# Kernel tuning notes

Measured on AMD Instinct MI355X. Metric: run time of the kernel, lower is better.

The kernel has to match this reference:

```python
import jax, jax.numpy as jnp
import numpy as np
import math

N_HEADS = 8
EPS = 1e-12


def _ln(x, g, b):
    m = x.mean(-1, keepdims=True)
    v = ((x - m) ** 2).mean(-1, keepdims=True)
    return (x - m) * jax.lax.rsqrt(v + EPS) * g + b


def _ffn(x, w1, b1, w2, b2):
    # torch nn.GELU default = exact erf gelu; dropout is identity in eval
    return jax.nn.gelu(x @ w1 + b1, approximate=False) @ w2 + b2


def _mha(q_in, kv, mask, qw, qb, kw, kb, vw, vb, ow, ob):
    B, S, _ = q_in.shape
    dh = qw.shape[1] // N_HEADS

    def split(x):
        return x.reshape(B, S, N_HEADS, dh).transpose(0, 2, 1, 3)  # (B,H,S,dh)

    q = split(q_in @ qw + qb) / math.sqrt(dh)
    k = split(kv @ kw + kb)
    v = split(kv @ vw + vb)
    scores = jnp.einsum('bhqd,bhkd->bhqk', q, k) + mask[:, None]
    w = jax.nn.softmax(scores, axis=-1)
    ctx = jnp.einsum('bhqk,bhkd->bhqd', w, v)
    ctx = ctx.transpose(0, 2, 1, 3).reshape(B, S, N_HEADS * dh)
    return ctx @ ow + ob


def reference(hidden, lens,
              f_ffn_w1, f_ffn_b1, f_ffn_w2, f_ffn_b2, f_ln_g, f_ln_b,
              f_q_w, f_q_b, f_k_w, f_k_b, f_v_w, f_v_b, f_o_w, f_o_b,
              b_ffn_w1, b_ffn_b1, b_ffn_w2, b_ffn_b2, b_ln_g, b_ln_b,
              b_q_w, b_q_b, b_k_w, b_k_b, b_v_w, b_v_b, b_o_w, b_o_b,
              attn_ln_g, attn_ln_b,
              out_ffn_w1, out_ffn_b1, out_ffn_w2, out_ffn_b2,
              out_ln_g, out_ln_b):
    S, B, D2 = hidden.shape
    H = D2 // 2
    S2 = S - 2
    f = hidden[..., :H]
    bk = hidden[..., H:]
    query = jnp.concatenate([f[:-2], bk[2:]], axis=-1)        # (S2, B, 2H)
    qbf = jnp.swapaxes(query, 0, 1)                            # (B, S2, 2H)

    # vectorized per-sample length-dependent masks (additive, 0 / -inf)
    qi = jnp.arange(S2)[:, None]
    ki = jnp.arange(S2)[None, :]
    Lm = (lens - 2)[:, None, None]
    # forward: rows >= L-2 all zero; valid rows causal (k <= q) inside [0, L-2)
    f_mask = jnp.where((qi >= Lm) | (ki <= qi), 0.0, -np.inf).astype(hidden.dtype)
    # backward: rows >= L-2 all zero; valid rows anti-causal (k >= q) with k < L-2
    b_mask = jnp.where((qi >= Lm) | ((ki >= qi) & (ki < Lm)), 0.0, -np.inf).astype(hidden.dtype)

    f_q = _ln(_ffn(qbf, f_ffn_w1, f_ffn_b1, f_ffn_w2, f_ffn_b2), f_ln_g, f_ln_b)
    f_kv = jnp.swapaxes(f[:-2], 0, 1)
    f_attn = _mha(f_q, f_kv, f_mask, f_q_w, f_q_b, f_k_w, f_k_b, f_v_w, f_v_b, f_o_w, f_o_b)

    b_q = _ln(_ffn(qbf, b_ffn_w1, b_ffn_b1, b_ffn_w2, b_ffn_b2), b_ln_g, b_ln_b)
    b_kv = jnp.swapaxes(bk[2:], 0, 1)
    b_attn = _mha(b_q, b_kv, b_mask, b_q_w, b_q_b, b_k_w, b_k_b, b_v_w, b_v_b, b_o_w, b_o_b)

    attn_out = _ln(qbf + jnp.concatenate([f_attn, b_attn], axis=-1), attn_ln_g, attn_ln_b)
    out = _ln(_ffn(attn_out, out_ffn_w1, out_ffn_b1, out_ffn_w2, out_ffn_b2), out_ln_g, out_ln_b)
    return jnp.swapaxes(out, 0, 1)                             # (S2, B, 2H)


def setup_inputs():
    key = jax.random.key(0)
    ks = jax.random.split(key, 16)
    S, B, H = 1024, 8, 512
    d = {}
    d['hidden'] = jax.random.normal(ks[0], (S, B, 2 * H), jnp.float32)
    d['lens'] = jax.random.randint(ks[1], (B,), 4, S + 1)

    def w(k, i, o):
        return jax.random.normal(k, (i, o), jnp.float32) * 0.02

    idx = 2
    for p in ('f', 'b'):
        d[p + '_ffn_w1'] = w(ks[idx], 2 * H, 2 * H); idx += 1
        d[p + '_ffn_b1'] = jnp.zeros((2 * H,), jnp.float32)
        d[p + '_ffn_w2'] = w(ks[idx], 2 * H, H); idx += 1
        d[p + '_ffn_b2'] = jnp.zeros((H,), jnp.float32)
        d[p + '_ln_g'] = jnp.ones((H,), jnp.float32)
        d[p + '_ln_b'] = jnp.zeros((H,), jnp.float32)
        for n in ('q', 'k', 'v', 'o'):
            d[p + '_' + n + '_w'] = w(jax.random.fold_in(ks[idx], hash(n) % 97), H, H)
            d[p + '_' + n + '_b'] = jnp.zeros((H,), jnp.float32)
        idx += 1
    d['attn_ln_g'] = jnp.ones((2 * H,), jnp.float32)
    d['attn_ln_b'] = jnp.zeros((2 * H,), jnp.float32)
    d['out_ffn_w1'] = w(ks[idx], 2 * H, 2 * H); idx += 1
    d['out_ffn_b1'] = jnp.zeros((2 * H,), jnp.float32)
    d['out_ffn_w2'] = w(ks[idx], 2 * H, 2 * H); idx += 1
    d['out_ffn_b2'] = jnp.zeros((2 * H,), jnp.float32)
    d['out_ln_g'] = jnp.ones((2 * H,), jnp.float32)
    d['out_ln_b'] = jnp.zeros((2 * H,), jnp.float32)
    return d
```

## Files before the change

### kernel.cpp

```cpp
#include <hip/hip_runtime.h>
#include <cmath>

#define S_ 1024
#define B_ 8
#define H_ 512
#define S2_ 1022
#define M_ (B_*S2_)
#define PAD_ 8192
#define VTS_ ((size_t)8*8*64*1024)

typedef __attribute__((ext_vector_type(8))) short bf16x8;
typedef __attribute__((ext_vector_type(4))) float f32x4;
typedef __attribute__((ext_vector_type(4))) unsigned int u32x4;
typedef __attribute__((ext_vector_type(2))) unsigned int u32x2;

__device__ __forceinline__ unsigned short f2bf(float f){
  unsigned int u = __float_as_uint(f);
  return (unsigned short)((u + 0x7fffu + ((u>>16)&1u)) >> 16);
}
__device__ __forceinline__ float bf2f(unsigned short u){
  return __uint_as_float((unsigned int)u << 16);
}
__device__ __forceinline__ float fgelu(float x){
  float u = x * (0.7978845608f + 0.0356774081f * x * x);
  return x / (1.f + __expf(-2.f * u));
}
__device__ __forceinline__ float fexp2(float x){
  float r; asm("v_exp_f32 %0, %1" : "=v"(r) : "v"(x)); return r;
}
__device__ __forceinline__ unsigned int cvtpk(float lo, float hi){
  unsigned int r; asm("v_cvt_pk_bf16_f32 %0, %1, %2" : "=v"(r) : "v"(lo), "v"(hi)); return r;
}

__device__ __forceinline__ void glds16(const void* g, void* l){
  __builtin_amdgcn_global_load_lds((const __attribute__((address_space(1))) unsigned int*)g,
                                   (__attribute__((address_space(3))) unsigned int*)l, 16, 0, 0);
}
#define SB() __builtin_amdgcn_sched_barrier(0)

__global__ __launch_bounds__(256) void lma_prep_x(const float* __restrict__ hidden,
                                                  unsigned short* __restrict__ Xb){
  int m = blockIdx.x; int dq = threadIdx.x * 4;
  int b = m / S2_, s = m - b * S2_;
  int srow = (dq < 512) ? s : (s + 2);
  const float* src = hidden + ((size_t)srow * B_ + b) * 1024 + dq;
  f32x4 v = *(const f32x4*)src;
  union { u32x2 u; unsigned short s4[4]; } pk;
  #pragma unroll
  for (int j = 0; j < 4; j++) pk.s4[j] = f2bf(v[j]);
  *(u32x2*)&Xb[(size_t)m * 1024 + dq] = pk.u;
}

struct TPack {
  const float* src[14];
  unsigned short* dst[14];
  int K[14];
  int N[14];
};
__global__ __launch_bounds__(256) void lma_transpose_all(TPack p){
  int idx = blockIdx.z;
  int K = p.K[idx], N = p.N[idx];
  int kb = blockIdx.x * 32, nb = blockIdx.y * 32;
  if (kb >= K || nb >= N) return;
  const float* W = p.src[idx];
  unsigned short* WT = p.dst[idx];
  __shared__ float t[32][33];
  int tx = threadIdx.x & 31, ty = threadIdx.x >> 5;
  #pragma unroll
  for (int i = ty; i < 32; i += 8) t[i][tx] = W[(size_t)(kb + i) * N + nb + tx];
  __syncthreads();
  #pragma unroll
  for (int i = ty; i < 32; i += 8) WT[(size_t)(nb + i) * K + kb + tx] = f2bf(t[tx][i]);
}

__global__ __launch_bounds__(256) void lma_biascat(const float* __restrict__ fk, const float* __restrict__ fv,
                                                   const float* __restrict__ bk, const float* __restrict__ bv,
                                                   float* __restrict__ out){
  int i = blockIdx.x * 256 + threadIdx.x;
  int fb = i >> 10, col = i & 1023;
  const float* s = (col < 512) ? (fb ? bk : fk) : (fb ? bv : fv);
  out[i] = s[col & 511];
}

__global__ __launch_bounds__(256) void lma_vt2(const unsigned short* __restrict__ KV2,
                                               unsigned short* __restrict__ VT2){
  __shared__ unsigned short t[32][34];
  int s0 = blockIdx.x * 32, c0 = blockIdx.y * 32;
  int z = blockIdx.z, fb = z >> 3, b = z & 7;
  const unsigned short* V = KV2 + (size_t)fb * PAD_ * 1024 + 512;
  unsigned short* VT = VT2 + (size_t)fb * VTS_;
  int tx = threadIdx.x & 31, ty = threadIdx.x >> 5;
  #pragma unroll
  for (int i = ty; i < 32; i += 8){
    int s = s0 + i; if (s > S2_-1) s = S2_-1;
    t[i][tx] = V[((size_t)b * S2_ + s) * 1024 + c0 + tx];
  }
  __syncthreads();
  int s = s0 + tx;
  #pragma unroll
  for (int i = ty; i < 32; i += 8){
    int c = c0 + i, h = c >> 6, d = c & 63;
    VT[(((size_t)b * 8 + h) * 64 + d) * 1024 + s] = (s < S2_) ? t[tx][i] : (unsigned short)0;
  }
}

__global__ __launch_bounds__(256) void lma_gemm2(
    const unsigned short* __restrict__ A, int lda,
    const unsigned short* __restrict__ Bt0, const unsigned short* __restrict__ Bt1,
    const float* __restrict__ bias0, const float* __restrict__ bias1,
    void* __restrict__ Cout, int ldc,
    int M, int N, int K, int mode, int amap, int nmt)
{
  __shared__ unsigned short Al[128*32];
  __shared__ unsigned short Bl[128*32];
  const int tid = threadIdx.x;
  const int w = tid >> 6, lane = tid & 63, quad = lane >> 4, l16 = lane & 15;
  const int mt = blockIdx.x % nmt, nt = blockIdx.x / nmt;
  const int m0 = mt * 128, n0 = nt * 128;
  const int brch = m0 >> 13;
  const unsigned short* Bt = brch ? Bt1 : Bt0;
  const float* bias = brch ? bias1 : bias0;
  const int coloff = (amap == 2 && brch) ? 512 : 0;
  const int wm = (w >> 1) * 64, wn = (w & 1) * 64;

  f32x4 acc[4][4];
  #pragma unroll
  for (int i = 0; i < 4; i++)
    #pragma unroll
    for (int f = 0; f < 4; f++) acc[i][f] = f32x4{0.f,0.f,0.f,0.f};

  const int srow = lane >> 2;
  const int spc  = (((lane & 3) ^ ((lane >> 3) & 3))) * 8;
  const int rswz = (l16 >> 1) & 3;

  for (int k0 = 0; k0 < K; k0 += 32) {
    #pragma unroll
    for (int c = 0; c < 2; c++) {
      int ra = w*32 + c*16 + srow;
      int ga = m0 + ra;
      int ar;
      if (amap == 0) { ar = (ga > M-1) ? (M-1) : ga; }
      else { ar = ga & (PAD_-1); if (ar > M_-1) ar = M_-1; }
      glds16(A + (size_t)ar * lda + coloff + k0 + spc, &Al[(w*32 + c*16) * 32]);
      int gb = n0 + ra; if (gb > N-1) gb = N-1;
      glds16(Bt + (size_t)gb * K + k0 + spc, &Bl[(w*32 + c*16) * 32]);
    }
    __syncthreads();
    bf16x8 af[4], bfr[4];
    #pragma unroll
    for (int i = 0; i < 4; i++) af[i]  = *(const bf16x8*)&Al[(wm + i*16 + l16)*32 + ((quad ^ rswz) * 8)];
    #pragma unroll
    for (int f = 0; f < 4; f++) bfr[f] = *(const bf16x8*)&Bl[(wn + f*16 + l16)*32 + ((quad ^ rswz) * 8)];
    #pragma unroll
    for (int i = 0; i < 4; i++)
      #pragma unroll
      for (int f = 0; f < 4; f++)
        acc[i][f] = __builtin_amdgcn_mfma_f32_16x16x32_bf16(af[i], bfr[f], acc[i][f], 0, 0, 0);
    __syncthreads();
  }

  float bv[4];
  #pragma unroll
  for (int f = 0; f < 4; f++) bv[f] = bias ? bias[n0 + wn + f*16 + l16] : 0.f;
  const int col0 = n0 + wn + l16;
  #pragma unroll
  for (int i = 0; i < 4; i++) {
    #pragma unroll
    for (int r = 0; r < 4; r++) {
      int row = m0 + wm + i*16 + quad*4 + r;
      if (row < M) {
        #pragma unroll
        for (int f = 0; f < 4; f++) {
          float v = acc[i][f][r] + bv[f];
          if (mode == 2) v = fgelu(v);
          else if (mode == 1) v *= 0.18033688011112042f;
          if (mode <= 2) ((unsigned short*)Cout)[(size_t)row * ldc + col0 + f*16] = f2bf(v);
          else if (mode == 3) ((float*)Cout)[(size_t)row * ldc + col0 + f*16] = v;
          else {
            int sr = row % S2_, bb2 = row / S2_;
            ((float*)Cout)[((size_t)sr * B_ + bb2) * ldc + col0 + f*16] = v;
          }
        }
      }
    }
  }
}

__global__ __launch_bounds__(512, 2) void lma_gemm8(
    const unsigned short* __restrict__ A, int lda,
    const unsigned short* __restrict__ Bt0, const unsigned short* __restrict__ Bt1,
    const float* __restrict__ bias0, const float* __restrict__ bias1,
    unsigned short* __restrict__ Cout, int ldc,
    int M, int N, int K, int mode, int amap, int nmt)
{
  __shared__ unsigned short Ls[2][2][256*64];
  const int tid = threadIdx.x;
  const int w = tid >> 6, lane = tid & 63, quad = lane >> 4, l16 = lane & 15;
  const int mt = blockIdx.x % nmt, nt = blockIdx.x / nmt;
  const int m0 = mt * 256, n0 = nt * 256;
  const int brch = m0 >> 13;
  const unsigned short* Bt = brch ? Bt1 : Bt0;
  const float* bias = brch ? bias1 : bias0;
  const int coloff = (amap == 2 && brch) ? 512 : 0;
  const int wm = (w >> 2) * 128, wn = (w & 3) * 64;

  f32x4 acc[8][4];
  #pragma unroll
  for (int i = 0; i < 8; i++)
    #pragma unroll
    for (int f = 0; f < 4; f++) acc[i][f] = f32x4{0.f,0.f,0.f,0.f};

  const int lrow8 = lane >> 3;
  const int lkb   = lane & 7;
  const int NT = K >> 6;

  const unsigned short* aP[2][2]; const unsigned short* bP[2][2];
  int aD[2][2], bD[2][2];
  #pragma unroll
  for (int hf = 0; hf < 2; hf++)
    #pragma unroll
    for (int c = 0; c < 2; c++) {
      int rtA = (w>>2)*128 + hf*64 + ((w&3)*2 + c)*8 + lrow8;
      int kbA = lkb ^ (rtA & 7);
      int ga = m0 + rtA;
      int ar;
      if (amap == 0) { ar = (ga > M-1) ? (M-1) : ga; }
      else { ar = ga & (PAD_-1); if (ar > M_-1) ar = M_-1; }
      aP[hf][c] = A + (size_t)ar * lda + coloff + kbA*8;
      aD[hf][c] = ((w>>2)*128 + hf*64 + ((w&3)*2 + c)*8) * 64;
      int rtB = (w>>1)*64 + hf*32 + ((w&1)*2 + c)*8 + lrow8;
      int kbB = lkb ^ (rtB & 7);
      int gb = n0 + rtB; if (gb > N-1) gb = N-1;
      bP[hf][c] = Bt + (size_t)gb * K + kbB*8;
      bD[hf][c] = ((w>>1)*64 + hf*32 + ((w&1)*2 + c)*8) * 64;
    }

  bf16x8 af[4][2], bf[2][2];

  #define STA(buf, hf, kt) { _Pragma("unroll") for (int c = 0; c < 2; c++) \
      glds16(aP[hf][c] + (size_t)(kt)*64, &Ls[buf][0][aD[hf][c]]); }
  #define STB(buf, hf, kt) { _Pragma("unroll") for (int c = 0; c < 2; c++) \
      glds16(bP[hf][c] + (size_t)(kt)*64, &Ls[buf][1][bD[hf][c]]); }
  #define LDA8(buf, mq) { _Pragma("unroll") for (int j = 0; j < 4; j++){ \
      int rt = wm + (mq)*64 + j*16 + l16; \
      const unsigned short* base = &Ls[buf][0][rt*64]; \
      int f_ = rt & 7; \
      af[j][0] = *(const bf16x8*)(base + ((    quad) ^ f_)*8); \
      af[j][1] = *(const bf16x8*)(base + ((4 + quad) ^ f_)*8); } }
  #define LDB8(buf, nq) { _Pragma("unroll") for (int j = 0; j < 2; j++){ \
      int rt = wn + (nq)*32 + j*16 + l16; \
      const unsigned short* base = &Ls[buf][1][rt*64]; \
      int f_ = rt & 7; \
      bf[j][0] = *(const bf16x8*)(base + ((    quad) ^ f_)*8); \
      bf[j][1] = *(const bf16x8*)(base + ((4 + quad) ^ f_)*8); } }
  #define MFMAQ(mq, nq) { __builtin_amdgcn_s_setprio(1); \
      _Pragma("unroll") for (int j = 0; j < 4; j++) \
        _Pragma("unroll") for (int j2 = 0; j2 < 2; j2++){ \
          acc[(mq)*4+j][(nq)*2+j2] = __builtin_amdgcn_mfma_f32_16x16x32_bf16(af[j][0], bf[j2][0], acc[(mq)*4+j][(nq)*2+j2], 0, 0, 0); \
          acc[(mq)*4+j][(nq)*2+j2] = __builtin_amdgcn_mfma_f32_16x16x32_bf16(af[j][1], bf[j2][1], acc[(mq)*4+j][(nq)*2+j2], 0, 0, 0); } \
      __builtin_amdgcn_s_setprio(0); }
  #define BAR()   { SB(); __builtin_amdgcn_s_barrier(); SB(); }
  #define LGKM0() { asm volatile("s_waitcnt lgkmcnt(0)" ::: "memory"); SB(); }
  #define VM6()   { asm volatile("s_waitcnt vmcnt(6)"   ::: "memory"); SB(); }
  #define VM2()   { asm volatile("s_waitcnt vmcnt(2)"   ::: "memory"); SB(); }

  STA(0, 0, 0); STB(0, 0, 0); STB(0, 1, 0); STA(0, 1, 0);
  STA(1, 0, 1);
  asm volatile("s_waitcnt vmcnt(2)" ::: "memory"); SB();
  BAR();

  const int NI = NT >> 1;
  for (int i = 0; i < NI; i++) {
    const int tb  = 2*i + 1;
    int ta2 = 2*i + 2; if (ta2 > NT-1) ta2 = NT-1;
    int tb2 = 2*i + 3; if (tb2 > NT-1) tb2 = NT-1;

    LDA8(0, 0); LDB8(0, 0); STB(1, 0, tb);
    BAR(); LGKM0(); MFMAQ(0, 0); BAR();
    LDB8(0, 1); STB(1, 1, tb);
    BAR(); LGKM0(); MFMAQ(0, 1); BAR();
    LDA8(0, 1); STA(1, 1, tb);
    BAR(); LGKM0(); MFMAQ(1, 1); BAR();
    LDB8(0, 0); STA(0, 0, ta2);
    BAR(); LGKM0(); MFMAQ(1, 0); VM6(); BAR();
    LDA8(1, 0); LDB8(1, 0); STB(0, 1, ta2);
    BAR(); LGKM0(); MFMAQ(0, 0); VM6(); BAR();
    LDB8(1, 1); STA(0, 1, ta2);
    BAR(); LGKM0(); MFMAQ(0, 1); VM6(); BAR();
    LDA8(1, 1); STB(0, 0, ta2);
    BAR(); LGKM0(); MFMAQ(1, 1); BAR();
    LDB8(1, 0); STA(1, 0, tb2);
    BAR(); LGKM0(); MFMAQ(1, 0); VM2(); BAR();
  }
  asm volatile("s_waitcnt vmcnt(0)" ::: "memory");

  float bv[4];
  #pragma unroll
  for (int f = 0; f < 4; f++) bv[f] = bias ? bias[n0 + wn + f*16 + l16] : 0.f;
  const int col0 = n0 + wn + l16;
  #pragma unroll
  for (int i2 = 0; i2 < 8; i2++) {
    #pragma unroll
    for (int r = 0; r < 4; r++) {
      int row = m0 + wm + i2*16 + quad*4 + r;
      if (row < M) {
        #pragma unroll
        for (int f = 0; f < 4; f++) {
          float v = acc[i2][f][r] + bv[f];
          if (mode == 2) v = fgelu(v);
          Cout[(size_t)row * ldc + col0 + f*16] = f2bf(v);
        }
      }
    }
  }
  #undef STA
  #undef STB
  #undef LDA8
  #undef LDB8
  #undef MFMAQ
  #undef BAR
  #undef LGKM0
  #undef VM6
  #undef VM2
}

__device__ __forceinline__ void lma_red2(float& s, float& sq){
  __shared__ float red[16];
  #pragma unroll
  for (int msk = 1; msk < 64; msk <<= 1){ s += __shfl_xor(s, msk); sq += __shfl_xor(sq, msk); }
  int w = threadIdx.x >> 6;
  if ((threadIdx.x & 63) == 0){ red[w] = s; red[8 + w] = sq; }
  __syncthreads();
  s  = red[0] + red[1] + red[2] + red[3];
  sq = red[8] + red[9] + red[10] + red[11];
}

__global__ __launch_bounds__(256) void lma_ln(const float* __restrict__ in,
                                              const float* __restrict__ g, const float* __restrict__ bb,
                                              int D, unsigned short* __restrict__ obf, float* __restrict__ of32){
  int row = blockIdx.x, t = threadIdx.x;
  const float* x = in + (size_t)row * D;
  float s = 0.f, sq = 0.f;
  for (int d = t; d < D; d += 256){ float v = x[d]; s += v; sq += v * v; }
  lma_red2(s, sq);
  float mean = s / D;
  float var = sq / D - mean * mean;
  float rstd = rsqrtf(fmaxf(var, 0.f) + 1e-12f);
  if (obf) {
    for (int d = t; d < D; d += 256) obf[(size_t)row * D + d] = f2bf((x[d] - mean) * rstd * g[d] + bb[d]);
  } else {
    for (int d = t; d < D; d += 256) of32[(size_t)row * D + d] = (x[d] - mean) * rstd * g[d] + bb[d];
  }
}

__global__ __launch_bounds__(256) void lma_ln2(const unsigned short* __restrict__ T12b,
                                               const float* __restrict__ fg, const float* __restrict__ fbb,
                                               const float* __restrict__ bg, const float* __restrict__ bbb,
                                               unsigned short* __restrict__ LQ2){
  int m = blockIdx.x, t = threadIdx.x;
  int fb = (m >= M_);
  int idx = m - fb * M_;
  const float* g = fb ? bg : fg;
  const float* bb = fb ? bbb : fbb;
  const unsigned short* x = T12b + ((size_t)fb * PAD_ + idx) * 512;
  unsigned short* o = LQ2 + ((size_t)fb * PAD_ + idx) * 512;
  float v0 = bf2f(x[t]), v1 = bf2f(x[t + 256]);
  float s = v0 + v1, sq = v0*v0 + v1*v1;
  lma_red2(s, sq);
  float mean = s / 512.f;
  float var = sq / 512.f - mean * mean;
  float rstd = rsqrtf(fmaxf(var, 0.f) + 1e-12f);
  o[t]       = f2bf((v0 - mean) * rstd * g[t]       + bb[t]);
  o[t + 256] = f2bf((v1 - mean) * rstd * g[t + 256] + bb[t + 256]);
}

__global__ __launch_bounds__(256) void lma_attn_ln(const unsigned short* __restrict__ pf,
                                                   const unsigned short* __restrict__ pb,
                                                   const float* __restrict__ hidden,
                                                   const float* __restrict__ g, const float* __restrict__ bb,
                                                   unsigned short* __restrict__ out){
  int m = blockIdx.x, t = threadIdx.x;
  int b = m / S2_, s = m - b * S2_;
  const float* hf = hidden + ((size_t)s       * B_ + b) * 1024;
  const float* hb = hidden + ((size_t)(s + 2) * B_ + b) * 1024;
  float v[4]; float sum = 0.f, sq = 0.f;
  #pragma unroll
  for (int j = 0; j < 4; j++){
    int d = t + j * 256;
    float x = (d < 512) ? (bf2f(pf[(size_t)m * 512 + d]) + hf[d])
                        : (bf2f(pb[(size_t)m * 512 + (d - 512)]) + hb[d]);
    v[j] = x; sum += x; sq += x * x;
  }
  lma_red2(sum, sq);
  float mean = sum / 1024.f;
  float var = sq / 1024.f - mean * mean;
  float rstd = rsqrtf(fmaxf(var, 0.f) + 1e-12f);
  #pragma unroll
  for (int j = 0; j < 4; j++){
    int d = t + j * 256;
    out[(size_t)m * 1024 + d] = f2bf((v[j] - mean) * rstd * g[d] + bb[d]);
  }
}

__global__ __launch_bounds__(256, 4) void lma_attn9(const unsigned short* __restrict__ Q2,
                                                    const unsigned short* __restrict__ KV2,
                                                    const unsigned short* __restrict__ VT2,
                                                    unsigned short* __restrict__ CT2,
                                                    const int* __restrict__ lens,
                                                    int fb){
  __shared__ unsigned short Kl[64*64];
  __shared__ unsigned short Vl[64*64];
  __shared__ __align__(16) unsigned short Pl[4][16*64];

  const int tid = threadIdx.x;
  const int w = tid >> 6, lane = tid & 63, quad = lane >> 4, l16 = lane & 15;
  const int id = blockIdx.x;
  const int qt = id >> 6, h = (id >> 3) & 7, b = id & 7;
  const int backward = fb;
  const int L2 = lens[b] - 2;
  const int q0wg = qt * 64;
  const int q0 = q0wg + w * 16;
  const int qg = q0 + l16;
  const int qload = (qg > S2_-1) ? (S2_-1) : qg;

  const size_t qbase  = ((size_t)b * S2_) * 512  + h * 64;
  const size_t kbase  = ((size_t)b * S2_) * 1024 + h * 64;
  const size_t vtbase = ((size_t)(b * 8 + h) * 64) * 1024;
  char* Pb = (char*)&Pl[w][0];

  const int lrow = lane >> 3;
  const int g0s  = (lane & 7) ^ lrow;
  const int x7   = l16 & 7;
  const int x7s  = x7 << 4;

  const unsigned short* Q  = Q2  + (size_t)fb * PAD_ * 512;
  const unsigned short* Kx = KV2 + (size_t)fb * PAD_ * 1024;
  const unsigned short* VT = VT2 + (size_t)fb * VTS_;
  unsigned short* CTX      = CT2 + (size_t)fb * PAD_ * 512;

  bf16x8 qf[2];
  {
    const unsigned short* qp = Q + qbase + (size_t)qload * 512 + quad * 8;
    qf[0] = *(const bf16x8*)(qp);
    qf[1] = *(const bf16x8*)(qp + 32);
  }

  float mi = -3e38f, li = 0.f;
  f32x4 ot[4];
  #pragma unroll
  for (int f = 0; f < 4; f++) ot[f] = f32x4{0.f,0.f,0.f,0.f};

  int klo = 0, khi = S2_ - 1;
  if (q0wg + 63 < L2) {
    if (!backward) khi = q0wg + 63;
    else { klo = q0wg; khi = L2 - 1; }
  }

  for (int kt0 = klo; kt0 <= khi; kt0 += 64) {
    #pragma unroll
    for (int c = 0; c < 2; c++) {
      int r = w*16 + c*8 + lrow;
      int kr = kt0 + r; if (kr > S2_-1) kr = S2_-1;
      glds16(Kx + kbase + (size_t)kr * 1024 + g0s * 8, &Kl[(w*16 + c*8) * 64]);
      glds16(VT + vtbase + (size_t)r * 1024 + kt0 + g0s * 8, &Vl[(w*16 + c*8) * 64]);
    }
    __syncthreads();

    bf16x8 kf[4][2], vf[4][2];
    #pragma unroll
    for (int sub = 0; sub < 4; sub++) {
      const unsigned short* kp = &Kl[(sub*16 + l16) * 64];
      kf[sub][0] = *(const bf16x8*)(kp + (( quad      ^ x7) * 8));
      kf[sub][1] = *(const bf16x8*)(kp + (((quad + 4) ^ x7) * 8));
    }
    #pragma unroll
    for (int f = 0; f < 4; f++) {
      const unsigned short* vp = &Vl[(f*16 + l16) * 64];
      vf[f][0] = *(const bf16x8*)(vp + (( quad      ^ x7) * 8));
      vf[f][1] = *(const bf16x8*)(vp + (((quad + 4) ^ x7) * 8));
    }

    f32x4 st[4];
    __builtin_amdgcn_s_setprio(1);
    #pragma unroll
    for (int sub = 0; sub < 4; sub++) {
      f32x4 s = f32x4{0.f,0.f,0.f,0.f};
      s = __builtin_amdgcn_mfma_f32_16x16x32_bf16(kf[sub][0], qf[0], s, 0, 0, 0);
      s = __builtin_amdgcn_mfma_f32_16x16x32_bf16(kf[sub][1], qf[1], s, 0, 0, 0);
      st[sub] = s;
    }
    __builtin_amdgcn_s_setprio(0);

    {
      bool tail = (kt0 + 63 > S2_ - 1);
      bool full;
      if (!backward) full = !tail && ((kt0 + 63 <= q0) || (q0 >= L2));
      else           full = !tail && ((q0 >= L2) || ((kt0 >= q0 + 15) && (kt0 + 63 < L2)));
      if (!full) {
        #pragma unroll
        for (int sub = 0; sub < 4; sub++) {
          #pragma unroll
          for (int r = 0; r < 4; r++) {
            int kg = kt0 + sub*16 + quad*4 + r;
            bool ok;
            if (!backward) ok = (kg < S2_) && ((qg >= L2) || (kg <= qg));
            else           ok = (kg < S2_) && ((qg >= L2) || ((kg >= qg) && (kg < L2)));
            if (!ok) st[sub][r] = -3e38f;
          }
        }
      }
    }

    float mx = -3e38f;
    #pragma unroll
    for (int sub = 0; sub < 4; sub++)
      #pragma unroll
      for (int r = 0; r < 4; r++) mx = fmaxf(mx, st[sub][r]);
    mx = fmaxf(mx, __shfl_xor(mx, 16));
    mx = fmaxf(mx, __shfl_xor(mx, 32));

    if (__any(mx > mi + 11.f)) {
      float mn = fmaxf(mi, mx);
      float al = fexp2(mi - mn);
      li *= al;
      #pragma unroll
      for (int f = 0; f < 4; f++)
        #pragma unroll
        for (int r = 0; r < 4; r++) ot[f][r] *= al;
      mi = mn;
    }

    float rs = 0.f;
    #pragma unroll
    for (int sub = 0; sub < 4; sub++)
      #pragma unroll
      for (int r = 0; r < 4; r++) {
        float p = fexp2(st[sub][r] - mi);
        st[sub][r] = p; rs += p;
      }
    rs += __shfl_xor(rs, 16);
    rs += __shfl_xor(rs, 32);
    li += rs;

    #pragma unroll
    for (int sub = 0; sub < 4; sub++) {
      u32x2 pk2;
      pk2[0] = cvtpk(st[sub][0], st[sub][1]);
      pk2[1] = cvtpk(st[sub][2], st[sub][3]);
      *(u32x2*)(Pb + (l16*128 + ((sub*32 + quad*8) ^ x7s))) = pk2;
    }
    bf16x8 pfr0 = *(const bf16x8*)(Pb + (l16*128 + (( 0 + quad*16) ^ x7s)));
    bf16x8 pfr1 = *(const bf16x8*)(Pb + (l16*128 + ((64 + quad*16) ^ x7s)));

    __builtin_amdgcn_s_setprio(1);
    #pragma unroll
    for (int f = 0; f < 4; f++) {
      ot[f] = __builtin_amdgcn_mfma_f32_16x16x32_bf16(vf[f][0], pfr0, ot[f], 0, 0, 0);
      ot[f] = __builtin_amdgcn_mfma_f32_16x16x32_bf16(vf[f][1], pfr1, ot[f], 0, 0, 0);
    }
    __builtin_amdgcn_s_setprio(0);
    __syncthreads();
  }

  if (qg < S2_) {
    float rcp = 1.f / li;
    #pragma unroll
    for (int f = 0; f < 4; f++) {
      ushort4 pk;
      pk.x = f2bf(ot[f][0] * rcp); pk.y = f2bf(ot[f][1] * rcp);
      pk.z = f2bf(ot[f][2] * rcp); pk.w = f2bf(ot[f][3] * rcp);
      *(ushort4*)&CTX[qbase + (size_t)qg * 512 + f*16 + quad*4] = pk;
    }
  }
}

extern "C" void kernel_launch(void* const* d_in, const int* in_sizes, int n_in,
                              void* d_out, int out_size, void* d_ws, size_t ws_size,
                              hipStream_t stream)
{
  const float* hidden = (const float*)d_in[0];
  const int*   lens   = (const int*)d_in[1];
  const float* fw[14]; for (int i = 0; i < 14; i++) fw[i] = (const float*)d_in[2 + i];
  const float* bw[14]; for (int i = 0; i < 14; i++) bw[i] = (const float*)d_in[16 + i];
  const float* attn_g = (const float*)d_in[30];
  const float* attn_b = (const float*)d_in[31];
  const float* o_w1 = (const float*)d_in[32];
  const float* o_b1 = (const float*)d_in[33];
  const float* o_w2 = (const float*)d_in[34];
  const float* o_b2 = (const float*)d_in[35];
  const float* o_lng = (const float*)d_in[36];
  const float* o_lnb = (const float*)d_in[37];

  char* ws = (char*)d_ws;
  size_t off = 0;
  auto alloc = [&](size_t bytes)->char* {
    off = (off + 255) & ~(size_t)255;
    char* p = ws + off; off += bytes; return p;
  };

  unsigned short* fw1t = (unsigned short*)alloc((size_t)1024*1024*2);
  unsigned short* fw2t = (unsigned short*)alloc((size_t)512*1024*2);
  unsigned short* fqt  = (unsigned short*)alloc((size_t)512*512*2);
  unsigned short* fkvt = (unsigned short*)alloc((size_t)1024*512*2);
  unsigned short* fot  = (unsigned short*)alloc((size_t)512*512*2);
  unsigned short* bw1t = (unsigned short*)alloc((size_t)1024*1024*2);
  unsigned short* bw2t = (unsigned short*)alloc((size_t)512*1024*2);
  unsigned short* bqt  = (unsigned short*)alloc((size_t)512*512*2);
  unsigned short* bkvt = (unsigned short*)alloc((size_t)1024*512*2);
  unsigned short* bot  = (unsigned short*)alloc((size_t)512*512*2);
  unsigned short* ow1t = (unsigned short*)alloc((size_t)1024*1024*2);
  unsigned short* ow2t = (unsigned short*)alloc((size_t)1024*1024*2);
  float*          biasKV = (float*)alloc(2048*4);

  unsigned short* Xb   = (unsigned short*)alloc((size_t)M_*1024*2);
  unsigned short* big1 = (unsigned short*)alloc((size_t)2*PAD_*1024*2);
  float*          big2 = (float*)alloc((size_t)2*PAD_*512*4);
  unsigned short* LQCT = (unsigned short*)alloc((size_t)2*PAD_*512*2);
  unsigned short* Q2   = (unsigned short*)alloc((size_t)2*PAD_*512*2);

  unsigned short* H12 = big1, *KV2 = big1, *H1o = big1;
  unsigned short* T12b = (unsigned short*)big2;
  unsigned short* VT2  = (unsigned short*)big2;
  unsigned short* P2b  = (unsigned short*)big2 + 2*VTS_;
  unsigned short* LQ2 = LQCT, *CT2 = LQCT;

  lma_prep_x<<<M_, 256, 0, stream>>>(hidden, Xb);

  {
    TPack tp;
    const float* srcs[14] = { fw[0], fw[2], fw[6], fw[8], fw[10], fw[12],
                              bw[0], bw[2], bw[6], bw[8], bw[10], bw[12],
                              o_w1, o_w2 };
    unsigned short* dsts[14] = { fw1t, fw2t, fqt, fkvt, fkvt + (size_t)512*512, fot,
                                 bw1t, bw2t, bqt, bkvt, bkvt + (size_t)512*512, bot,
                                 ow1t, ow2t };
    int Ks[14] = {1024,1024,512,512,512,512, 1024,1024,512,512,512,512, 1024,1024};
    int Ns[14] = {1024, 512,512,512,512,512, 1024, 512,512,512,512,512, 1024,1024};
    for (int i = 0; i < 14; i++){ tp.src[i]=srcs[i]; tp.dst[i]=dsts[i]; tp.K[i]=Ks[i]; tp.N[i]=Ns[i]; }
    lma_transpose_all<<<dim3(32, 32, 14), 256, 0, stream>>>(tp);
  }
  lma_biascat<<<8, 256, 0, stream>>>(fw[9], fw[11], bw[9], bw[11], biasKV);

  auto G = [&](const unsigned short* A, int lda,
               const unsigned short* B0, const unsigned short* B1,
               const float* b0, const float* b1,
               void* C, int ldc, int M, int N, int K, int mode, int amap){
    int nmt = (M + 127) / 128;
    lma_gemm2<<<dim3(nmt * (N/128)), 256, 0, stream>>>(A, lda, B0, B1, b0, b1, C, ldc, M, N, K, mode, amap, nmt);
  };
  auto G8 = [&](const unsigned short* A, int lda,
                const unsigned short* B0, const unsigned short* B1,
                const float* b0, const float* b1,
                unsigned short* C, int ldc, int M, int N, int K, int mode, int amap){
    int nmt = M / 256;
    lma_gemm8<<<dim3(nmt * (N/256)), 512, 0, stream>>>(A, lda, B0, B1, b0, b1, C, ldc, M, N, K, mode, amap, nmt);
  };

  G8(Xb, 1024, fw1t, bw1t, fw[1], bw[1], H12, 1024, 2*PAD_, 1024, 1024, 2, 1);
  G(H12, 1024, fw2t, bw2t, fw[3], bw[3], T12b, 512, 2*PAD_, 512, 1024, 0, 0);
  lma_ln2<<<2*M_, 256, 0, stream>>>(T12b, fw[4], fw[5], bw[4], bw[5], LQ2);
  G(LQ2, 512, fqt, bqt, fw[7], bw[7], Q2, 512, 2*PAD_, 512, 512, 1, 0);
  G8(Xb, 1024, fkvt, bkvt, biasKV, biasKV + 1024, KV2, 1024, 2*PAD_, 1024, 512, 0, 2);
  lma_vt2<<<dim3(32, 16, 16), 256, 0, stream>>>(KV2, VT2);

  lma_attn9<<<dim3(1024), 256, 0, stream>>>(Q2, KV2, VT2, CT2, lens, 0);
  lma_attn9<<<dim3(1024), 256, 0, stream>>>(Q2, KV2, VT2, CT2, lens, 1);

  G(CT2, 512, fot, bot, fw[13], bw[13], P2b, 512, 2*PAD_, 512, 512, 0, 0);

  lma_attn_ln<<<M_, 256, 0, stream>>>(P2b, P2b + (size_t)PAD_*512, hidden, attn_g, attn_b, Xb);

  G(Xb, 1024, ow1t, ow1t, o_b1, o_b1, H1o, 1024, M_, 1024, 1024, 2, 0);
  G(H1o, 1024, ow2t, ow2t, o_b2, o_b2, (float*)d_out, 1024, M_, 1024, 1024, 4, 0);
  lma_ln<<<M_, 256, 0, stream>>>((float*)d_out, o_lng, o_lnb, 1024, nullptr, (float*)d_out);
}
```

Measured before the change: 568.9 us.

## Add 128x256 eight-wave GEMM kernel for remaining GEMMs and merge attention directions

Adds a new 512-thread GEMM kernel with 128x256 tiles, a double-buffered LDS pipeline and interleaved load/MFMA phases. It replaces the older 128x128 lma_gemm2 path for the FFN2, Q projection, output projection and output FFN GEMMs. Separately, forward and backward attention now run sequentially inside one launch instead of two. The wider tiles aim to raise operand reuse and per-block MFMA throughput, at the cost of higher register/LDS use per block. Serialising the two directions per block halves the grid's parallel work in exchange for one fewer launch.

Measured after the change: 550.8 us. 3.2% less time.

```diff
diff --git a/kernel.cpp b/kernel.cpp
--- a/kernel.cpp
+++ b/kernel.cpp
@@ -324,6 +324,146 @@
   #undef VM2
 }
 
+__global__ __launch_bounds__(512, 2) void lma_gemm8w(
+    const unsigned short* __restrict__ A, int lda,
+    const unsigned short* __restrict__ Bt0, const unsigned short* __restrict__ Bt1,
+    const float* __restrict__ bias0, const float* __restrict__ bias1,
+    void* __restrict__ Cout, int ldc,
+    int M, int N, int K, int mode, int nmt)
+{
+  __shared__ unsigned short LsA[2][128*64];
+  __shared__ unsigned short LsB[2][256*64];
+  const int tid = threadIdx.x;
+  const int w = tid >> 6, lane = tid & 63, quad = lane >> 4, l16 = lane & 15;
+  const int mt = blockIdx.x % nmt, nt = blockIdx.x / nmt;
+  const int m0 = mt * 128, n0 = nt * 256;
+  const int brch = m0 >> 13;
+  const unsigned short* Bt = brch ? Bt1 : Bt0;
+  const float* bias = brch ? bias1 : bias0;
+  const int wm = (w >> 2) * 64, wn = (w & 3) * 64;
+
+  f32x4 acc[4][4];
+  #pragma unroll
+  for (int i = 0; i < 4; i++)
+    #pragma unroll
+    for (int f = 0; f < 4; f++) acc[i][f] = f32x4{0.f,0.f,0.f,0.f};
+
+  const int lrow8 = lane >> 3;
+  const int lkb   = lane & 7;
+  const int NT = K >> 6;
+
+  const unsigned short* aP[2]; int aD[2];
+  const unsigned short* bP[2][2]; int bD[2][2];
+  #pragma unroll
+  for (int hf = 0; hf < 2; hf++) {
+    int rtA = hf*64 + w*8 + lrow8;
+    int kbA = lkb ^ (rtA & 7);
+    int ga = m0 + rtA; if (ga > M-1) ga = M-1;
+    aP[hf] = A + (size_t)ga * lda + kbA*8;
+    aD[hf] = (hf*64 + w*8) * 64;
+    #pragma unroll
+    for (int c = 0; c < 2; c++) {
+      int rtB = hf*128 + (w*2 + c)*8 + lrow8;
+      int kbB = lkb ^ (rtB & 7);
+      int gb = n0 + rtB; if (gb > N-1) gb = N-1;
+      bP[hf][c] = Bt + (size_t)gb * K + kbB*8;
+      bD[hf][c] = (hf*128 + (w*2 + c)*8) * 64;
+    }
+  }
+
+  bf16x8 af[2][2], bf[2][2];
+
+  #define WSTA(buf, hf, kt) { glds16(aP[hf] + (size_t)(kt)*64, &LsA[buf][aD[hf]]); }
+  #define WSTB(buf, hf, kt) { _Pragma("unroll") for (int c = 0; c < 2; c++) \
+      glds16(bP[hf][c] + (size_t)(kt)*64, &LsB[buf][bD[hf][c]]); }
+  #define WLDA(buf, mq) { _Pragma("unroll") for (int j = 0; j < 2; j++){ \
+      int rt = wm + (mq)*32 + j*16 + l16; \
+      const unsigned short* base = &LsA[buf][rt*64]; \
+      int f_ = rt & 7; \
+      af[j][0] = *(const bf16x8*)(base + ((    quad) ^ f_)*8); \
+      af[j][1] = *(const bf16x8*)(base + ((4 + quad) ^ f_)*8); } }
+  #define WLDB(buf, nq) { _Pragma("unroll") for (int j = 0; j < 2; j++){ \
+      int rt = wn + (nq)*32 + j*16 + l16; \
+      const unsigned short* base = &LsB[buf][rt*64]; \
+      int f_ = rt & 7; \
+      bf[j][0] = *(const bf16x8*)(base + ((    quad) ^ f_)*8); \
+      bf[j][1] = *(const bf16x8*)(base + ((4 + quad) ^ f_)*8); } }
+  #define WMFMAQ(mq, nq) { __builtin_amdgcn_s_setprio(1); \
+      _Pragma("unroll") for (int j = 0; j < 2; j++) \
+        _Pragma("unroll") for (int j2 = 0; j2 < 2; j2++){ \
+          acc[(mq)*2+j][(nq)*2+j2] = __builtin_amdgcn_mfma_f32_16x16x32_bf16(af[j][0], bf[j2][0], acc[(mq)*2+j][(nq)*2+j2], 0, 0, 0); \
+          acc[(mq)*2+j][(nq)*2+j2] = __builtin_amdgcn_mfma_f32_16x16x32_bf16(af[j][1], bf[j2][1], acc[(mq)*2+j][(nq)*2+j2], 0, 0, 0); } \
+      __builtin_amdgcn_s_setprio(0); }
+  #define WBAR()   { SB(); __builtin_amdgcn_s_barrier(); SB(); }
+  #define WLGKM0() { asm volatile("s_waitcnt lgkmcnt(0)" ::: "memory"); SB(); }
+  #define WVM4()   { asm volatile("s_waitcnt vmcnt(4)"   ::: "memory"); SB(); }
+  #define WVM1()   { asm volatile("s_waitcnt vmcnt(1)"   ::: "memory"); SB(); }
+
+  WSTA(0, 0, 0); WSTB(0, 0, 0); WSTB(0, 1, 0); WSTA(0, 1, 0);
+  WSTA(1, 0, 1);
+  WVM1(); WBAR();
+
+  const int NI = NT >> 1;
+  for (int i = 0; i < NI; i++) {
+    const int tb  = 2*i + 1;
+    int ta2 = 2*i + 2; if (ta2 > NT-1) ta2 = NT-1;
+    int tb2 = 2*i + 3; if (tb2 > NT-1) tb2 = NT-1;
+
+    WLDA(0, 0); WLDB(0, 0); WSTB(1, 0, tb);
+    WBAR(); WLGKM0(); WMFMAQ(0, 0); WBAR();
+    WLDB(0, 1); WSTB(1, 1, tb);
+    WBAR(); WLGKM0(); WMFMAQ(0, 1); WBAR();
+    WLDA(0, 1); WSTA(1, 1, tb);
+    WBAR(); WLGKM0(); WMFMAQ(1, 1); WBAR();
+    WLDB(0, 0); WSTA(0, 0, ta2);
+    WBAR(); WLGKM0(); WMFMAQ(1, 0); WVM4(); WBAR();
+    WLDA(1, 0); WLDB(1, 0); WSTB(0, 1, ta2);
+    WBAR(); WLGKM0(); WMFMAQ(0, 0); WVM4(); WBAR();
+    WLDB(1, 1); WSTA(0, 1, ta2);
+    WBAR(); WLGKM0(); WMFMAQ(0, 1); WVM4(); WBAR();
+    WLDA(1, 1); WSTB(0, 0, ta2);
+    WBAR(); WLGKM0(); WMFMAQ(1, 1); WBAR();
+    WLDB(1, 0); WSTA(1, 0, tb2);
+    WBAR(); WLGKM0(); WMFMAQ(1, 0); WVM1(); WBAR();
+  }
+  asm volatile("s_waitcnt vmcnt(0)" ::: "memory");
+
+  float bv[4];
+  #pragma unroll
+  for (int f = 0; f < 4; f++) bv[f] = bias ? bias[n0 + wn + f*16 + l16] : 0.f;
+  const int col0 = n0 + wn + l16;
+  #pragma unroll
+  for (int i2 = 0; i2 < 4; i2++) {
+    #pragma unroll
+    for (int r = 0; r < 4; r++) {
+      int row = m0 + wm + i2*16 + quad*4 + r;
+      if (row < M) {
+        #pragma unroll
+        for (int f = 0; f < 4; f++) {
+          float v = acc[i2][f][r] + bv[f];
+          if (mode == 2) v = fgelu(v);
+          else if (mode == 1) v *= 0.18033688011112042f;
+          if (mode <= 2) ((unsigned short*)Cout)[(size_t)row * ldc + col0 + f*16] = f2bf(v);
+          else if (mode == 3) ((float*)Cout)[(size_t)row * ldc + col0 + f*16] = v;
+          else {
+            int sr = row % S2_, bb2 = row / S2_;
+            ((float*)Cout)[((size_t)sr * B_ + bb2) * ldc + col0 + f*16] = v;
+          }
+        }
+      }
+    }
+  }
+  #undef WSTA
+  #undef WSTB
+  #undef WLDA
+  #undef WLDB
+  #undef WMFMAQ
+  #undef WBAR
+  #undef WLGKM0
+  #undef WVM4
+  #undef WVM1
+}
+
 __device__ __forceinline__ void lma_red2(float& s, float& sq){
   __shared__ float red[16];
   #pragma unroll
@@ -402,12 +542,11 @@
   }
 }
 
-__global__ __launch_bounds__(256, 4) void lma_attn9(const unsigned short* __restrict__ Q2,
-                                                    const unsigned short* __restrict__ KV2,
-                                                    const unsigned short* __restrict__ VT2,
-                                                    unsigned short* __restrict__ CT2,
-                                                    const int* __restrict__ lens,
-                                                    int fb){
+__global__ __launch_bounds__(256, 4) void lma_attn10(const unsigned short* __restrict__ Q2,
+                                                     const unsigned short* __restrict__ KV2,
+                                                     const unsigned short* __restrict__ VT2,
+                                                     unsigned short* __restrict__ CT2,
+                                                     const int* __restrict__ lens){
   __shared__ unsigned short Kl[64*64];
   __shared__ unsigned short Vl[64*64];
   __shared__ __align__(16) unsigned short Pl[4][16*64];
@@ -416,7 +555,6 @@
   const int w = tid >> 6, lane = tid & 63, quad = lane >> 4, l16 = lane & 15;
   const int id = blockIdx.x;
   const int qt = id >> 6, h = (id >> 3) & 7, b = id & 7;
-  const int backward = fb;
   const int L2 = lens[b] - 2;
   const int q0wg = qt * 64;
   const int q0 = q0wg + w * 16;
@@ -433,143 +571,146 @@
   const int x7   = l16 & 7;
   const int x7s  = x7 << 4;
 
-  const unsigned short* Q  = Q2  + (size_t)fb * PAD_ * 512;
-  const unsigned short* Kx = KV2 + (size_t)fb * PAD_ * 1024;
-  const unsigned short* VT = VT2 + (size_t)fb * VTS_;
-  unsigned short* CTX      = CT2 + (size_t)fb * PAD_ * 512;
-
-  bf16x8 qf[2];
-  {
-    const unsigned short* qp = Q + qbase + (size_t)qload * 512 + quad * 8;
-    qf[0] = *(const bf16x8*)(qp);
-    qf[1] = *(const bf16x8*)(qp + 32);
-  }
-
-  float mi = -3e38f, li = 0.f;
-  f32x4 ot[4];
-  #pragma unroll
-  for (int f = 0; f < 4; f++) ot[f] = f32x4{0.f,0.f,0.f,0.f};
-
-  int klo = 0, khi = S2_ - 1;
-  if (q0wg + 63 < L2) {
-    if (!backward) khi = q0wg + 63;
-    else { klo = q0wg; khi = L2 - 1; }
-  }
-
-  for (int kt0 = klo; kt0 <= khi; kt0 += 64) {
-    #pragma unroll
-    for (int c = 0; c < 2; c++) {
-      int r = w*16 + c*8 + lrow;
-      int kr = kt0 + r; if (kr > S2_-1) kr = S2_-1;
-      glds16(Kx + kbase + (size_t)kr * 1024 + g0s * 8, &Kl[(w*16 + c*8) * 64]);
-      glds16(VT + vtbase + (size_t)r * 1024 + kt0 + g0s * 8, &Vl[(w*16 + c*8) * 64]);
-    }
-    __syncthreads();
-
-    bf16x8 kf[4][2], vf[4][2];
-    #pragma unroll
-    for (int sub = 0; sub < 4; sub++) {
-      const unsigned short* kp = &Kl[(sub*16 + l16) * 64];
-      kf[sub][0] = *(const bf16x8*)(kp + (( quad      ^ x7) * 8));
-      kf[sub][1] = *(const bf16x8*)(kp + (((quad + 4) ^ x7) * 8));
-    }
-    #pragma unroll
-    for (int f = 0; f < 4; f++) {
-      const unsigned short* vp = &Vl[(f*16 + l16) * 64];
-      vf[f][0] = *(const bf16x8*)(vp + (( quad      ^ x7) * 8));
-      vf[f][1] = *(const bf16x8*)(vp + (((quad + 4) ^ x7) * 8));
-    }
-
-    f32x4 st[4];
-    __builtin_amdgcn_s_setprio(1);
-    #pragma unroll
-    for (int sub = 0; sub < 4; sub++) {
-      f32x4 s = f32x4{0.f,0.f,0.f,0.f};
-      s = __builtin_amdgcn_mfma_f32_16x16x32_bf16(kf[sub][0], qf[0], s, 0, 0, 0);
-      s = __builtin_amdgcn_mfma_f32_16x16x32_bf16(kf[sub][1], qf[1], s, 0, 0, 0);
-      st[sub] = s;
-    }
-    __builtin_amdgcn_s_setprio(0);
-
+  for (int fb = 0; fb < 2; fb++) {
+    const int backward = fb;
+    const unsigned short* Q  = Q2  + (size_t)fb * PAD_ * 512;
+    const unsigned short* Kx = KV2 + (size_t)fb * PAD_ * 1024;
+    const unsigned short* VT = VT2 + (size_t)fb * VTS_;
+    unsigned short* CTX      = CT2 + (size_t)fb * PAD_ * 512;
+
+    bf16x8 qf[2];
     {
-      bool tail = (kt0 + 63 > S2_ - 1);
-      bool full;
-      if (!backward) full = !tail && ((kt0 + 63 <= q0) || (q0 >= L2));
-      else           full = !tail && ((q0 >= L2) || ((kt0 >= q0 + 15) && (kt0 + 63 < L2)));
-      if (!full) {
-        #pragma unroll
-        for (int sub = 0; sub < 4; sub++) {
+      const unsigned short* qp = Q + qbase + (size_t)qload * 512 + quad * 8;
+      qf[0] = *(const bf16x8*)(qp);
+      qf[1] = *(const bf16x8*)(qp + 32);
+    }
+
+    float mi = -3e38f, li = 0.f;
+    f32x4 ot[4];
+    #pragma unroll
+    for (int f = 0; f < 4; f++) ot[f] = f32x4{0.f,0.f,0.f,0.f};
+
+    int klo = 0, khi = S2_ - 1;
+    if (q0wg + 63 < L2) {
+      if (!backward) khi = q0wg + 63;
+      else { klo = q0wg; khi = L2 - 1; }
+    }
+
+    for (int kt0 = klo; kt0 <= khi; kt0 += 64) {
+      #pragma unroll
+      for (int c = 0; c < 2; c++) {
+        int r = w*16 + c*8 + lrow;
+        int kr = kt0 + r; if (kr > S2_-1) kr = S2_-1;
+        glds16(Kx + kbase + (size_t)kr * 1024 + g0s * 8, &Kl[(w*16 + c*8) * 64]);
+        glds16(VT + vtbase + (size_t)r * 1024 + kt0 + g0s * 8, &Vl[(w*16 + c*8) * 64]);
+      }
+      __syncthreads();
+
+      bf16x8 kf[4][2], vf[4][2];
+      #pragma unroll
+      for (int sub = 0; sub < 4; sub++) {
+        const unsigned short* kp = &Kl[(sub*16 + l16) * 64];
+        kf[sub][0] = *(const bf16x8*)(kp + (( quad      ^ x7) * 8));
+        kf[sub][1] = *(const bf16x8*)(kp + (((quad + 4) ^ x7) * 8));
+      }
+      #pragma unroll
+      for (int f = 0; f < 4; f++) {
+        const unsigned short* vp = &Vl[(f*16 + l16) * 64];
+        vf[f][0] = *(const bf16x8*)(vp + (( quad      ^ x7) * 8));
+        vf[f][1] = *(const bf16x8*)(vp + (((quad + 4) ^ x7) * 8));
+      }
+
+      f32x4 st[4];
+      __builtin_amdgcn_s_setprio(1);
+      #pragma unroll
+      for (int sub = 0; sub < 4; sub++) {
+        f32x4 s = f32x4{0.f,0.f,0.f,0.f};
+        s = __builtin_amdgcn_mfma_f32_16x16x32_bf16(kf[sub][0], qf[0], s, 0, 0, 0);
+        s = __builtin_amdgcn_mfma_f32_16x16x32_bf16(kf[sub][1], qf[1], s, 0, 0, 0);
+        st[sub] = s;
+      }
+      __builtin_amdgcn_s_setprio(0);
+
+      {
+        bool tail = (kt0 + 63 > S2_ - 1);
+        bool full;
+        if (!backward) full = !tail && ((kt0 + 63 <= q0) || (q0 >= L2));
+        else           full = !tail && ((q0 >= L2) || ((kt0 >= q0 + 15) && (kt0 + 63 < L2)));
+        if (!full) {
           #pragma unroll
-          for (int r = 0; r < 4; r++) {
-            int kg = kt0 + sub*16 + quad*4 + r;
-            bool ok;
-            if (!backward) ok = (kg < S2_) && ((qg >= L2) || (kg <= qg));
-            else           ok = (kg < S2_) && ((qg >= L2) || ((kg >= qg) && (kg < L2)));
-            if (!ok) st[sub][r] = -3e38f;
+          for (int sub = 0; sub < 4; sub++) {
+            #pragma unroll
+            for (int r = 0; r < 4; r++) {
+              int kg = kt0 + sub*16 + quad*4 + r;
+              bool ok;
+              if (!backward) ok = (kg < S2_) && ((qg >= L2) || (kg <= qg));
+              else           ok = (kg < S2_) && ((qg >= L2) || ((kg >= qg) && (kg < L2)));
+              if (!ok) st[sub][r] = -3e38f;
+            }
           }
         }
       }
-    }
-
-    float mx = -3e38f;
-    #pragma unroll
-    for (int sub = 0; sub < 4; sub++)
-      #pragma unroll
-      for (int r = 0; r < 4; r++) mx = fmaxf(mx, st[sub][r]);
-    mx = fmaxf(mx, __shfl_xor(mx, 16));
-    mx = fmaxf(mx, __shfl_xor(mx, 32));
-
-    if (__any(mx > mi + 11.f)) {
-      float mn = fmaxf(mi, mx);
-      float al = fexp2(mi - mn);
-      li *= al;
-      #pragma unroll
-      for (int f = 0; f < 4; f++)
+
+      float mx = -3e38f;
+      #pragma unroll
+      for (int sub = 0; sub < 4; sub++)
         #pragma unroll
-        for (int r = 0; r < 4; r++) ot[f][r] *= al;
-      mi = mn;
-    }
-
-    float rs = 0.f;
-    #pragma unroll
-    for (int sub = 0; sub < 4; sub++)
-      #pragma unroll
-      for (int r = 0; r < 4; r++) {
-        float p = fexp2(st[sub][r] - mi);
-        st[sub][r] = p; rs += p;
-      }
-    rs += __shfl_xor(rs, 16);
-    rs += __shfl_xor(rs, 32);
-    li += rs;
-
-    #pragma unroll
-    for (int sub = 0; sub < 4; sub++) {
-      u32x2 pk2;
-      pk2[0] = cvtpk(st[sub][0], st[sub][1]);
-      pk2[1] = cvtpk(st[sub][2], st[sub][3]);
-      *(u32x2*)(Pb + (l16*128 + ((sub*32 + quad*8) ^ x7s))) = pk2;
-    }
-    bf16x8 pfr0 = *(const bf16x8*)(Pb + (l16*128 + (( 0 + quad*16) ^ x7s)));
-    bf16x8 pfr1 = *(const bf16x8*)(Pb + (l16*128 + ((64 + quad*16) ^ x7s)));
-
-    __builtin_amdgcn_s_setprio(1);
-    #pragma unroll
-    for (int f = 0; f < 4; f++) {
-      ot[f] = __builtin_amdgcn_mfma_f32_16x16x32_bf16(vf[f][0], pfr0, ot[f], 0, 0, 0);
-      ot[f] = __builtin_amdgcn_mfma_f32_16x16x32_bf16(vf[f][1], pfr1, ot[f], 0, 0, 0);
-    }
-    __builtin_amdgcn_s_setprio(0);
-    __syncthreads();
-  }
-
-  if (qg < S2_) {
-    float rcp = 1.f / li;
-    #pragma unroll
-    for (int f = 0; f < 4; f++) {
-      ushort4 pk;
-      pk.x = f2bf(ot[f][0] * rcp); pk.y = f2bf(ot[f][1] * rcp);
-      pk.z = f2bf(ot[f][2] * rcp); pk.w = f2bf(ot[f][3] * rcp);
-      *(ushort4*)&CTX[qbase + (size_t)qg * 512 + f*16 + quad*4] = pk;
+        for (int r = 0; r < 4; r++) mx = fmaxf(mx, st[sub][r]);
+      mx = fmaxf(mx, __shfl_xor(mx, 16));
+      mx = fmaxf(mx, __shfl_xor(mx, 32));
+
+      if (__any(mx > mi + 11.f)) {
+        float mn = fmaxf(mi, mx);
+        float al = fexp2(mi - mn);
+        li *= al;
+        #pragma unroll
+        for (int f = 0; f < 4; f++)
+          #pragma unroll
+          for (int r = 0; r < 4; r++) ot[f][r] *= al;
+        mi = mn;
+      }
+
+      float rs = 0.f;
+      #pragma unroll
+      for (int sub = 0; sub < 4; sub++)
+        #pragma unroll
+        for (int r = 0; r < 4; r++) {
+          float p = fexp2(st[sub][r] - mi);
+          st[sub][r] = p; rs += p;
+        }
+      rs += __shfl_xor(rs, 16);
+      rs += __shfl_xor(rs, 32);
+      li += rs;
+
+      #pragma unroll
+      for (int sub = 0; sub < 4; sub++) {
+        u32x2 pk2;
+        pk2[0] = cvtpk(st[sub][0], st[sub][1]);
+        pk2[1] = cvtpk(st[sub][2], st[sub][3]);
+        *(u32x2*)(Pb + (l16*128 + ((sub*32 + quad*8) ^ x7s))) = pk2;
+      }
+      bf16x8 pfr0 = *(const bf16x8*)(Pb + (l16*128 + (( 0 + quad*16) ^ x7s)));
+      bf16x8 pfr1 = *(const bf16x8*)(Pb + (l16*128 + ((64 + quad*16) ^ x7s)));
+
+      __builtin_amdgcn_s_setprio(1);
+      #pragma unroll
+      for (int f = 0; f < 4; f++) {
+        ot[f] = __builtin_amdgcn_mfma_f32_16x16x32_bf16(vf[f][0], pfr0, ot[f], 0, 0, 0);
+        ot[f] = __builtin_amdgcn_mfma_f32_16x16x32_bf16(vf[f][1], pfr1, ot[f], 0, 0, 0);
+      }
+      __builtin_amdgcn_s_setprio(0);
+      __syncthreads();
+    }
+
+    if (qg < S2_) {
+      float rcp = 1.f / li;
+      #pragma unroll
+      for (int f = 0; f < 4; f++) {
+        ushort4 pk;
+        pk.x = f2bf(ot[f][0] * rcp); pk.y = f2bf(ot[f][1] * rcp);
+        pk.z = f2bf(ot[f][2] * rcp); pk.w = f2bf(ot[f][3] * rcp);
+        *(ushort4*)&CTX[qbase + (size_t)qg * 512 + f*16 + quad*4] = pk;
+      }
     }
   }
 }
@@ -641,13 +782,6 @@
   }
   lma_biascat<<<8, 256, 0, stream>>>(fw[9], fw[11], bw[9], bw[11], biasKV);
 
-  auto G = [&](const unsigned short* A, int lda,
-               const unsigned short* B0, const unsigned short* B1,
-               const float* b0, const float* b1,
-               void* C, int ldc, int M, int N, int K, int mode, int amap){
-    int nmt = (M + 127) / 128;
-    lma_gemm2<<<dim3(nmt * (N/128)), 256, 0, stream>>>(A, lda, B0, B1, b0, b1, C, ldc, M, N, K, mode, amap, nmt);
-  };
   auto G8 = [&](const unsigned short* A, int lda,
                 const unsigned short* B0, const unsigned short* B1,
                 const float* b0, const float* b1,
@@ -655,22 +789,28 @@
     int nmt = M / 256;
     lma_gemm8<<<dim3(nmt * (N/256)), 512, 0, stream>>>(A, lda, B0, B1, b0, b1, C, ldc, M, N, K, mode, amap, nmt);
   };
+  auto G8W = [&](const unsigned short* A, int lda,
+                 const unsigned short* B0, const unsigned short* B1,
+                 const float* b0, const float* b1,
+                 void* C, int ldc, int M, int N, int K, int mode){
+    int nmt = (M + 127) / 128;
+    lma_gemm8w<<<dim3(nmt * (N/256)), 512, 0, stream>>>(A, lda, B0, B1, b0, b1, C, ldc, M, N, K, mode, nmt);
+  };
 
   G8(Xb, 1024, fw1t, bw1t, fw[1], bw[1], H12, 1024, 2*PAD_, 1024, 1024, 2, 1);
-  G(H12, 1024, fw2t, bw2t, fw[3], bw[3], T12b, 512, 2*PAD_, 512, 1024, 0, 0);
+  G8W(H12, 1024, fw2t, bw2t, fw[3], bw[3], T12b, 512, 2*PAD_, 512, 1024, 0);
   lma_ln2<<<2*M_, 256, 0, stream>>>(T12b, fw[4], fw[5], bw[4], bw[5], LQ2);
-  G(LQ2, 512, fqt, bqt, fw[7], bw[7], Q2, 512, 2*PAD_, 512, 512, 1, 0);
+  G8W(LQ2, 512, fqt, bqt, fw[7], bw[7], Q2, 512, 2*PAD_, 512, 512, 1);
   G8(Xb, 1024, fkvt, bkvt, biasKV, biasKV + 1024, KV2, 1024, 2*PAD_, 1024, 512, 0, 2);
   lma_vt2<<<dim3(32, 16, 16), 256, 0, stream>>>(KV2, VT2);
 
-  lma_attn9<<<dim3(1024), 256, 0, stream>>>(Q2, KV2, VT2, CT2, lens, 0);
-  lma_attn9<<<dim3(1024), 256, 0, stream>>>(Q2, KV2, VT2, CT2, lens, 1);
-
-  G(CT2, 512, fot, bot, fw[13], bw[13], P2b, 512, 2*PAD_, 512, 512, 0, 0);
+  lma_attn10<<<dim3(1024), 256, 0, stream>>>(Q2, KV2, VT2, CT2, lens);
+
+  G8W(CT2, 512, fot, bot, fw[13], bw[13], P2b, 512, 2*PAD_, 512, 512, 0);
 
   lma_attn_ln<<<M_, 256, 0, stream>>>(P2b, P2b + (size_t)PAD_*512, hidden, attn_g, attn_b, Xb);
 
-  G(Xb, 1024, ow1t, ow1t, o_b1, o_b1, H1o, 1024, M_, 1024, 1024, 2, 0);
-  G(H1o, 1024, ow2t, ow2t, o_b2, o_b2, (float*)d_out, 1024, M_, 1024, 1024, 4, 0);
+  G8W(Xb, 1024, ow1t, ow1t, o_b1, o_b1, H1o, 1024, M_, 1024, 1024, 2);
+  G8W(H1o, 1024, ow2t, ow2t, o_b2, o_b2, (float*)d_out, 1024, M_, 1024, 1024, 4);
   lma_ln<<<M_, 256, 0, stream>>>((float*)d_out, o_lng, o_lnb, 1024, nullptr, (float*)d_out);
 }
```
